# Optimization experiments

Measured on AMD Instinct MI355X. Metric: run time of the kernel, lower is better.

Reference implementation:

```python
import jax, jax.numpy as jnp
import numpy as np

DN = ('NCDHW', 'OIDHW', 'NCDHW')


def conv3d(x, w, b, stride=2, pad=1):
    # w: [Cout, Cin, k, k, k] (PyTorch Conv3d layout == OIDHW)
    y = jax.lax.conv_general_dilated(x, w, (stride,) * 3, [(pad, pad)] * 3,
                                     dimension_numbers=DN)
    return y + b[None, :, None, None, None]


def convT3d(x, w, b, stride=2, pad=1):
    # w: [Cin, Cout, k, k, k] (PyTorch ConvTranspose3d layout).
    # ConvTranspose(k,s,p) == conv(lhs_dilated by s, flipped kernel, pad = k-1-p)
    k = w.shape[2]
    wf = jnp.transpose(jnp.flip(w, (2, 3, 4)), (1, 0, 2, 3, 4))  # -> OIDHW
    p = k - 1 - pad
    y = jax.lax.conv_general_dilated(x, wf, (1, 1, 1), [(p, p)] * 3,
                                     lhs_dilation=(stride,) * 3,
                                     dimension_numbers=DN)
    return y + b[None, :, None, None, None]


def setup_inputs() -> dict:
    key = jax.random.key(0)
    ks = jax.random.split(key, 14)
    s = 0.05
    inp = {
        'x': jax.random.normal(ks[0], (4, 1, 128, 128, 128), jnp.float32),
        # encoder conv weights (OIDHW) + biases
        'w1': jax.random.normal(ks[1], (16, 1, 4, 4, 4), jnp.float32) * s,
        'b1': jnp.zeros((16,), jnp.float32),
        'w2': jax.random.normal(ks[2], (32, 16, 4, 4, 4), jnp.float32) * s,
        'b2': jnp.zeros((32,), jnp.float32),
        'w3': jax.random.normal(ks[3], (64, 32, 4, 4, 4), jnp.float32) * s,
        'b3': jnp.zeros((64,), jnp.float32),
        # VQ codebook [num_embeddings=512, latent_dim=64]
        'codebook': jax.random.normal(ks[4], (512, 64), jnp.float32),
        # decoder conv-transpose weights (PyTorch layout: [Cin, Cout, k,k,k]) + biases
        'dw1': jax.random.normal(ks[5], (64, 32, 4, 4, 4), jnp.float32) * s,
        'db1': jnp.zeros((32,), jnp.float32),
        'dw2': jax.random.normal(ks[6], (32, 16, 4, 4, 4), jnp.float32) * s,
        'db2': jnp.zeros((16,), jnp.float32),
        'dw3': jax.random.normal(ks[7], (16, 1, 4, 4, 4), jnp.float32) * s,
        'db3': jnp.zeros((1,), jnp.float32),
    }
    return inp


def reference(x, w1, b1, w2, b2, w3, b3, codebook, dw1, db1, dw2, db2, dw3, db3):
    # ---- encoder ----
    h = jax.nn.relu(conv3d(x, w1, b1))
    h = jax.nn.relu(conv3d(h, w2, b2))
    z_e = conv3d(h, w3, b3)                      # [B, C=64, D, H, W]
    B, C, D, H, W = z_e.shape

    # ---- vector quantization (cdist + argmin + gather) ----
    zf = jnp.transpose(z_e.reshape(B, C, -1), (0, 2, 1))   # [B, N, C]
    # squared euclidean distances (argmin identical to cdist argmin)
    d2 = (jnp.sum(zf * zf, axis=-1, keepdims=True)
          + jnp.sum(codebook * codebook, axis=-1)[None, None, :]
          - 2.0 * jnp.einsum('bnc,kc->bnk', zf, codebook))  # [B, N, K]
    encoding_indices = jnp.argmin(d2, axis=-1)              # [B, N]
    q = codebook[encoding_indices]                          # [B, N, C]
    quantized = jnp.transpose(q, (0, 2, 1)).reshape(B, C, D, H, W)
    # straight-through estimator
    quantized = z_e + jax.lax.stop_gradient(quantized - z_e)

    # ---- decoder ----
    h = jax.nn.relu(convT3d(quantized, dw1, db1))
    h = jax.nn.relu(convT3d(h, dw2, db2))
    x_hat = jax.nn.sigmoid(convT3d(h, dw3, db3))
    return (x_hat, quantized, z_e)
```

## Files before the change

### kernel.cpp

```cpp
#include <hip/hip_runtime.h>
#include <math.h>


__device__ __forceinline__ float4 ld4(const float* p) {
  float4 q; __builtin_memcpy(&q, p, 16); return q;
}
struct F3 { float x, y, z; };
__device__ __forceinline__ F3 ld3(const float* p) {
  F3 q; __builtin_memcpy(&q, p, 12); return q;
}

#define WAVES_HINT __attribute__((amdgpu_waves_per_eu(2, 4)))

template<int CIN, int COUT>
__global__ __launch_bounds__(256) void k_repackT(const float* __restrict__ w,
                                                 float* __restrict__ dst) {
  const int idx = blockIdx.x * 256 + threadIdx.x;
  if (idx >= CIN * 8 * COUT * 8) return;
  const int a  = idx & 7;
  const int co = (idx >> 3) % COUT;
  const int p  = ((idx >> 3) / COUT) & 7;
  const int ci2 = idx / (8 * COUT * 8);
  const int az = a >> 2, ay = (a >> 1) & 1, ax = a & 1;
  const int pz = p >> 2, py = (p >> 1) & 1, px = p & 1;
  const int kz = 3 - pz - 2 * az, ky = 3 - py - 2 * ay, kx = 3 - px - 2 * ax;
  dst[(((size_t)(ci2 * 8 + p) * COUT + co) * 16) + az * 8 + (ay * 2 + ax)] =
      w[((size_t)ci2 * COUT + co) * 64 + (kz * 16 + ky * 4 + kx)];
}

template<int S, int D, int NCH>
__global__ __launch_bounds__(256) void k_zhalo(float* __restrict__ buf) {
  const int vol = S * S * S;
  const long long idx = (long long)blockIdx.x * 256 + threadIdx.x;
  if (idx >= (long long)NCH * vol) return;
  const int r = (int)(idx % vol);
  const int z = r / (S * S), y = (r / S) % S, x = r % S;
  if (z < 1 || z > D || y < 1 || y > D || x < 1 || x > D) buf[idx] = 0.0f;
}

__global__ __launch_bounds__(256) void k_pad(const float* __restrict__ x,
                                             float* __restrict__ dp) {
  constexpr long long VOL = 130LL * 130 * 130;
  const long long idx = (long long)blockIdx.x * 256 + threadIdx.x;
  if (idx >= 4 * VOL) return;
  const int b = (int)(idx / VOL);
  const int r = (int)(idx % VOL);
  const int z = r / (130 * 130), y = (r / 130) % 130, xx = r % 130;
  float v = 0.0f;
  if (z >= 1 && z <= 128 && y >= 1 && y <= 128 && xx >= 1 && xx <= 128)
    v = x[(((long long)b * 128 + (z - 1)) * 128 + (y - 1)) * 128 + (xx - 1)];
  dp[idx] = v;
}

template<int CIN, int COUT, int DIN, int DOUT, int OCG, int TZ, bool RELU,
         bool INP, int SIN, bool OUTP, int SOUT, int NG>
__global__ __launch_bounds__(256) WAVES_HINT
void k_conv(const float* __restrict__ xin, const float* __restrict__ wg,
            const float* __restrict__ bias, float* __restrict__ out) {
  constexpr int NBX = DOUT / 8, NBY = DOUT / 8, NBZ = DOUT / (4 * TZ);
  constexpr size_t VIN  = INP  ? (size_t)SIN * SIN * SIN : (size_t)DIN * DIN * DIN;
  constexpr size_t VOUT = OUTP ? (size_t)SOUT * SOUT * SOUT : (size_t)DOUT * DOUT * DOUT;
  const int tid = threadIdx.x;
  const int tx = tid & 7, ty = (tid >> 3) & 7, tz = tid >> 6;
  int bb = blockIdx.x;
  const int g  = bb % NG;  bb /= NG;
  const int gx = bb % NBX; bb /= NBX;
  const int gy = bb % NBY; bb /= NBY;
  const int gz = bb % NBZ; bb /= NBZ;
  const int b = bb;
  const int oc0 = g * OCG;
  const int ow = gx * 8 + tx, oh = gy * 8 + ty, od0 = gz * (4 * TZ) + tz;

  float acc[TZ][OCG];
#pragma unroll
  for (int j = 0; j < TZ; ++j)
#pragma unroll
    for (int c = 0; c < OCG; ++c) acc[j][c] = 0.0f;

#pragma unroll 1
  for (int ci = 0; ci < CIN; ++ci) {
    const float* xb = xin + (size_t)(b * CIN + ci) * VIN;
#pragma unroll 1
    for (int t16 = 0; t16 < 16; ++t16) {
      float4 q[TZ];
      if (INP) {
        const int zp = od0 * 2 + (t16 >> 2);
        const int yp = oh * 2 + (t16 & 3);
        const float* r0 = xb + ((size_t)zp * SIN + yp) * SIN + ow * 2;
#pragma unroll
        for (int j = 0; j < TZ; ++j) q[j] = ld4(r0 + (size_t)j * 8 * SIN * SIN);
      } else {
        const int y  = oh * 2 - 1 + (t16 & 3);
        const int x0 = ow * 2 - 1;
        const bool vy = (unsigned)y < (unsigned)DIN;
#pragma unroll
        for (int j = 0; j < TZ; ++j) {
          const int z = od0 * 2 - 1 + (t16 >> 2) + j * 8;
          const bool vz = vy && ((unsigned)z < (unsigned)DIN);
          const float* xr = xb + ((size_t)z * DIN + y) * DIN + x0;
          q[j].x = (vz && (unsigned)(x0 + 0) < (unsigned)DIN) ? xr[0] : 0.0f;
          q[j].y = (vz && (unsigned)(x0 + 1) < (unsigned)DIN) ? xr[1] : 0.0f;
          q[j].z = (vz && (unsigned)(x0 + 2) < (unsigned)DIN) ? xr[2] : 0.0f;
          q[j].w = (vz && (unsigned)(x0 + 3) < (unsigned)DIN) ? xr[3] : 0.0f;
        }
      }
#pragma unroll
      for (int c = 0; c < OCG; ++c) {
        const float4 w4 = ld4(wg + ((size_t)(oc0 + c) * CIN + ci) * 64 + t16 * 4);
#pragma unroll
        for (int j = 0; j < TZ; ++j) {
          acc[j][c] = fmaf(q[j].x, w4.x, acc[j][c]);
          acc[j][c] = fmaf(q[j].y, w4.y, acc[j][c]);
          acc[j][c] = fmaf(q[j].z, w4.z, acc[j][c]);
          acc[j][c] = fmaf(q[j].w, w4.w, acc[j][c]);
        }
      }
    }
  }

#pragma unroll
  for (int c = 0; c < OCG; ++c) {
    const float bv = bias[oc0 + c];
#pragma unroll
    for (int j = 0; j < TZ; ++j) {
      float v = acc[j][c] + bv;
      if (RELU) v = fmaxf(v, 0.0f);
      const int od = od0 + j * 4;
      if (OUTP)
        out[(size_t)(b * COUT + oc0 + c) * VOUT
            + ((size_t)(od + 1) * SOUT + (oh + 1)) * SOUT + (ow + 1)] = v;
      else
        out[(size_t)(b * COUT + oc0 + c) * VOUT
            + ((size_t)od * DOUT + oh) * DOUT + ow] = v;
    }
  }
}

template<int CIN, int COUT, int DIN, int OCG, int TZ, int EPI, int SIN,
         bool OUTP, int SOUT, int NG>
__global__ __launch_bounds__(256) WAVES_HINT
void k_convt(const float* __restrict__ xin, const float* __restrict__ wp,
             const float* __restrict__ bias, float* __restrict__ out) {
  constexpr int DOUT = 2 * DIN, NBX = DIN / 8, NBY = DIN / 8,
                NBZ = DIN / (4 * TZ);
  constexpr size_t VIN  = (size_t)SIN * SIN * SIN;
  constexpr size_t VOUT = OUTP ? (size_t)SOUT * SOUT * SOUT
                               : (size_t)DOUT * DOUT * DOUT;
  const int tid = threadIdx.x;
  const int tx = tid & 7, ty = (tid >> 3) & 7, tz = tid >> 6;
  int bb = blockIdx.x;
  const int g  = bb % NG;  bb /= NG;
  const int gx = bb % NBX; bb /= NBX;
  const int gy = bb % NBY; bb /= NBY;
  const int gz = bb % NBZ; bb /= NBZ;
  const int b = bb;
  const int oc0 = g * OCG;
  const int mx = gx * 8 + tx, my = gy * 8 + ty;
  const int mz0 = gz * (4 * TZ) + tz * TZ;

  float acc[TZ][8][OCG];
#pragma unroll
  for (int j = 0; j < TZ; ++j)
#pragma unroll
    for (int p = 0; p < 8; ++p)
#pragma unroll
      for (int c = 0; c < OCG; ++c) acc[j][p][c] = 0.0f;

#pragma unroll 1
  for (int ci = 0; ci < CIN; ++ci) {
    const float* xb = xin + (size_t)(b * CIN + ci) * VIN
                          + ((size_t)mz0 * SIN + my) * SIN + mx;
    float xn[TZ + 2][3][3];
#pragma unroll
    for (int dz = 0; dz < TZ + 2; ++dz)
#pragma unroll
      for (int dy = 0; dy < 3; ++dy) {
        const F3 t = ld3(xb + ((size_t)dz * SIN + dy) * SIN);
        xn[dz][dy][0] = t.x; xn[dz][dy][1] = t.y; xn[dz][dy][2] = t.z;
      }
    __builtin_amdgcn_sched_barrier(0);

    const float* wci = wp + (size_t)ci * 8 * COUT * 16;
#pragma unroll
    for (int p = 0; p < 8; ++p) {
      const int pz = p >> 2, py = (p >> 1) & 1, px = p & 1;
#pragma unroll
      for (int c = 0; c < OCG; ++c) {
        const float* wb = wci + ((size_t)p * COUT + (oc0 + c)) * 16;
        const float4 wA = ld4(wb);
        const float4 wB = ld4(wb + 8);
#pragma unroll
        for (int j = 0; j < TZ; ++j)
          acc[j][p][c] = fmaf(xn[j + pz][py    ][px    ], wA.x, acc[j][p][c]);
#pragma unroll
        for (int j = 0; j < TZ; ++j)
          acc[j][p][c] = fmaf(xn[j + pz][py    ][px + 1], wA.y, acc[j][p][c]);
#pragma unroll
        for (int j = 0; j < TZ; ++j)
          acc[j][p][c] = fmaf(xn[j + pz][py + 1][px    ], wA.z, acc[j][p][c]);
#pragma unroll
        for (int j = 0; j < TZ; ++j)
          acc[j][p][c] = fmaf(xn[j + pz][py + 1][px + 1], wA.w, acc[j][p][c]);
#pragma unroll
        for (int j = 0; j < TZ; ++j)
          acc[j][p][c] = fmaf(xn[j + pz + 1][py    ][px    ], wB.x, acc[j][p][c]);
#pragma unroll
        for (int j = 0; j < TZ; ++j)
          acc[j][p][c] = fmaf(xn[j + pz + 1][py    ][px + 1], wB.y, acc[j][p][c]);
#pragma unroll
        for (int j = 0; j < TZ; ++j)
          acc[j][p][c] = fmaf(xn[j + pz + 1][py + 1][px    ], wB.z, acc[j][p][c]);
#pragma unroll
        for (int j = 0; j < TZ; ++j)
          acc[j][p][c] = fmaf(xn[j + pz + 1][py + 1][px + 1], wB.w, acc[j][p][c]);
      }
    }
  }

#pragma unroll
  for (int c = 0; c < OCG; ++c) {
    const float bv = bias[oc0 + c];
#pragma unroll
    for (int j = 0; j < TZ; ++j) {
      const int mz = mz0 + j;
#pragma unroll
      for (int p = 0; p < 8; ++p) {
        const int pz = p >> 2, py = (p >> 1) & 1, px = p & 1;
        float v = acc[j][p][c] + bv;
        if (EPI == 1) v = fmaxf(v, 0.0f);
        if (EPI == 2) v = 1.0f / (1.0f + expf(-v));
        if (OUTP)
          out[(size_t)(b * COUT + oc0 + c) * VOUT
              + ((size_t)(2 * mz + pz + 1) * SOUT + (2 * my + py + 1)) * SOUT
              + (2 * mx + px + 1)] = v;
        else
          out[(size_t)(b * COUT + oc0 + c) * VOUT
              + ((size_t)(2 * mz + pz) * DOUT + (2 * my + py)) * DOUT
              + (2 * mx + px)] = v;
      }
    }
  }
}

__global__ __launch_bounds__(256) void k_vq(const float* __restrict__ ze,
                                            const float* __restrict__ cb,
                                            float* __restrict__ quant,
                                            float* __restrict__ quantp) {
  __shared__ float ct[64 * 65];
  __shared__ float zs[4][64];
  __shared__ int   bis[4];
  const int tid  = threadIdx.x;
  const int lane = tid & 63;
  const int wv   = tid >> 6;
  const int p0 = blockIdx.x * 4;
  const int b  = p0 >> 12;
  const int n0 = p0 & 4095;

  {
    const int c = tid >> 2, j = tid & 3;
    zs[j][c] = ze[((size_t)(b * 64 + c) << 12) + n0 + j];
  }

  float best = 3.4e38f;
  int bi = 0;
#pragma unroll 1
  for (int ch = 0; ch < 8; ++ch) {
    __syncthreads();
    for (int i = tid; i < 4096; i += 256) {
      const int r = i >> 6, c = i & 63;
      ct[r * 65 + c] = cb[((ch * 64 + r) << 6) + c];
    }
    __syncthreads();
    float d = 0.0f;
#pragma unroll 8
    for (int c = 0; c < 64; ++c) {
      const float t = zs[wv][c] - ct[lane * 65 + c];
      d = fmaf(t, t, d);
    }
    const int k = ch * 64 + lane;
    if (d < best) { best = d; bi = k; }
  }
#pragma unroll
  for (int off = 32; off > 0; off >>= 1) {
    const float ob = __shfl_down(best, off);
    const int   oi = __shfl_down(bi, off);
    if (ob < best || (ob == best && oi < bi)) { best = ob; bi = oi; }
  }
  if (lane == 0) bis[wv] = bi;
  __syncthreads();
  {
    const int c = tid >> 2, j = tid & 3;
    const float val = cb[(bis[j] << 6) + c];
    const int n = n0 + j;
    quant[((size_t)(b * 64 + c) << 12) + n] = val;
    const int zz = n >> 8, yy = (n >> 4) & 15, xx = n & 15;
    quantp[(size_t)(b * 64 + c) * 8000
           + ((size_t)(zz + 1) * 20 + (yy + 1)) * 20 + (xx + 1)] = val;
  }
}

extern "C" void kernel_launch(void* const* d_in, const int* in_sizes, int n_in,
                              void* d_out, int out_size, void* d_ws, size_t ws_size,
                              hipStream_t stream) {
  const float* x   = (const float*)d_in[0];
  const float* w1  = (const float*)d_in[1];
  const float* b1  = (const float*)d_in[2];
  const float* w2  = (const float*)d_in[3];
  const float* b2  = (const float*)d_in[4];
  const float* w3  = (const float*)d_in[5];
  const float* b3  = (const float*)d_in[6];
  const float* cb  = (const float*)d_in[7];
  const float* dw1 = (const float*)d_in[8];
  const float* db1 = (const float*)d_in[9];
  const float* dw2 = (const float*)d_in[10];
  const float* db2 = (const float*)d_in[11];
  const float* dw3 = (const float*)d_in[12];
  const float* db3 = (const float*)d_in[13];

  float* outf  = (float*)d_out;
  float* xhat  = outf;
  float* quant = outf + 8388608;
  float* ze    = outf + 9437184;

  float* dp = outf;

  float* regA = (float*)d_ws;
  float* regB = regA + (size_t)64 * 68 * 68 * 68;
  float* regC = regB + (size_t)128 * 36 * 36 * 36;
  float* t1p = regC + (size_t)256 * 20 * 20 * 20;
  float* t2p = t1p + 262144;
  float* t3p = t2p + 65536;

  k_repackT<64, 32><<<512, 256, 0, stream>>>(dw1, t1p);
  k_repackT<32, 16><<<128, 256, 0, stream>>>(dw2, t2p);
  k_repackT<16, 1><<<4, 256, 0, stream>>>(dw3, t3p);
  k_zhalo<68, 64, 64><<<78608, 256, 0, stream>>>(regA);
  k_zhalo<36, 32, 128><<<23328, 256, 0, stream>>>(regB);
  k_zhalo<20, 16, 256><<<8000, 256, 0, stream>>>(regC);
  k_pad<<<34329, 256, 0, stream>>>(x, dp);

  k_conv<1, 16, 128, 64, 16, 2, true, true, 130, true, 68, 1>
      <<<2048, 256, 0, stream>>>(dp, w1, b1, regA);
  k_conv<16, 32, 64, 32, 16, 1, true, true, 68, true, 36, 2>
      <<<1024, 256, 0, stream>>>(regA, w2, b2, regB);
  k_conv<32, 64, 32, 16, 4, 1, false, true, 36, false, 16, 16>
      <<<1024, 256, 0, stream>>>(regB, w3, b3, ze);
  k_vq<<<4096, 256, 0, stream>>>(ze, cb, quant, regC);
  k_convt<64, 32, 16, 2, 1, 1, 20, true, 36, 16>
      <<<1024, 256, 0, stream>>>(regC, t1p, db1, regB);
  k_convt<32, 16, 32, 2, 4, 1, 36, true, 68, 8>
      <<<1024, 256, 0, stream>>>(regB, t2p, db2, regA);
  k_convt<16, 1, 64, 1, 4, 2, 68, false, 0, 1>
      <<<1024, 256, 0, stream>>>(regA, t3p, db3, xhat);
}
```

Before: 1.060 ms.

## Stage conv and convT weights through double-buffered LDS with register prefetch

Both the strided conv and transposed conv kernels now copy each input channel's weight slice into shared memory once per block, with the next slice prefetched into registers while the current one is consumed. The inner loops then read weights from LDS instead of issuing per-thread global loads for the same uniform data. The cost is two block-wide barriers per input channel and extra LDS use, which may limit occupancy or stall waves.

```diff
diff --git a/kernel.cpp b/kernel.cpp
--- a/kernel.cpp
+++ b/kernel.cpp
@@ -60,6 +60,11 @@
   constexpr int NBX = DOUT / 8, NBY = DOUT / 8, NBZ = DOUT / (4 * TZ);
   constexpr size_t VIN  = INP  ? (size_t)SIN * SIN * SIN : (size_t)DIN * DIN * DIN;
   constexpr size_t VOUT = OUTP ? (size_t)SOUT * SOUT * SOUT : (size_t)DOUT * DOUT * DOUT;
+  constexpr int NBUF = (CIN > 1) ? 2 : 1;
+  constexpr int WPT  = (OCG * 64) / 256;
+  static_assert(WPT == 4 || WPT == 1, "OCG must be 16 or 4");
+  __shared__ float wlds[NBUF][OCG][64];
+
   const int tid = threadIdx.x;
   const int tx = tid & 7, ty = (tid >> 3) & 7, tz = tid >> 6;
   int bb = blockIdx.x;
@@ -71,14 +76,32 @@
   const int oc0 = g * OCG;
   const int ow = gx * 8 + tx, oh = gy * 8 + ty, od0 = gz * (4 * TZ) + tz;
 
+  const int s_oc  = (WPT == 4) ? (tid >> 4) : (tid >> 6);
+  const int s_off = (WPT == 4) ? ((tid & 15) << 2) : (tid & 63);
+
   float acc[TZ][OCG];
 #pragma unroll
   for (int j = 0; j < TZ; ++j)
 #pragma unroll
     for (int c = 0; c < OCG; ++c) acc[j][c] = 0.0f;
+
+  {
+    const float* src = wg + ((size_t)(oc0 + s_oc) * CIN + 0) * 64 + s_off;
+    if (WPT == 4) *(float4*)&wlds[0][s_oc][s_off] = ld4(src);
+    else          wlds[0][s_oc][s_off] = *src;
+  }
+  __syncthreads();
 
 #pragma unroll 1
   for (int ci = 0; ci < CIN; ++ci) {
+    float4 wpf4; float wpf1;
+    const bool pf = (CIN > 1) && (ci + 1 < CIN);
+    if (pf) {
+      const float* src = wg + ((size_t)(oc0 + s_oc) * CIN + (ci + 1)) * 64 + s_off;
+      if (WPT == 4) wpf4 = ld4(src); else wpf1 = *src;
+    }
+    const int cur = (CIN > 1) ? (ci & 1) : 0;
+
     const float* xb = xin + (size_t)(b * CIN + ci) * VIN;
 #pragma unroll 1
     for (int t16 = 0; t16 < 16; ++t16) {
@@ -106,7 +129,7 @@
       }
 #pragma unroll
       for (int c = 0; c < OCG; ++c) {
-        const float4 w4 = ld4(wg + ((size_t)(oc0 + c) * CIN + ci) * 64 + t16 * 4);
+        const float4 w4 = *(const float4*)&wlds[cur][c][t16 * 4];
 #pragma unroll
         for (int j = 0; j < TZ; ++j) {
           acc[j][c] = fmaf(q[j].x, w4.x, acc[j][c]);
@@ -115,6 +138,15 @@
           acc[j][c] = fmaf(q[j].w, w4.w, acc[j][c]);
         }
       }
+    }
+
+    if (CIN > 1) {
+      __syncthreads();
+      if (pf) {
+        if (WPT == 4) *(float4*)&wlds[cur ^ 1][s_oc][s_off] = wpf4;
+        else          wlds[cur ^ 1][s_oc][s_off] = wpf1;
+      }
+      __syncthreads();
     }
   }
 
@@ -146,6 +178,10 @@
   constexpr size_t VIN  = (size_t)SIN * SIN * SIN;
   constexpr size_t VOUT = OUTP ? (size_t)SOUT * SOUT * SOUT
                                : (size_t)DOUT * DOUT * DOUT;
+  constexpr int SL = 8 * OCG * 16;
+  static_assert(SL <= 256, "slice must fit one stage round");
+  __shared__ float wl[2][8][OCG][16];
+
   const int tid = threadIdx.x;
   const int tx = tid & 7, ty = (tid >> 3) & 7, tz = tid >> 6;
   int bb = blockIdx.x;
@@ -158,6 +194,11 @@
   const int mx = gx * 8 + tx, my = gy * 8 + ty;
   const int mz0 = gz * (4 * TZ) + tz * TZ;
 
+  const int s_p = tid / (OCG * 16);
+  const int s_c = (tid >> 4) % OCG;
+  const int s_f = tid & 15;
+  const float* wbase = wp + ((size_t)s_p * COUT + (oc0 + s_c)) * 16 + s_f;
+
   float acc[TZ][8][OCG];
 #pragma unroll
   for (int j = 0; j < TZ; ++j)
@@ -165,9 +206,17 @@
     for (int p = 0; p < 8; ++p)
 #pragma unroll
       for (int c = 0; c < OCG; ++c) acc[j][p][c] = 0.0f;
+
+  if (tid < SL) wl[0][s_p][s_c][s_f] = wbase[0];
+  __syncthreads();
 
 #pragma unroll 1
   for (int ci = 0; ci < CIN; ++ci) {
+    float wpf;
+    const bool pf = (ci + 1 < CIN);
+    if (pf && tid < SL) wpf = wbase[(size_t)(ci + 1) * 8 * COUT * 16];
+    const int cur = ci & 1;
+
     const float* xb = xin + (size_t)(b * CIN + ci) * VIN
                           + ((size_t)mz0 * SIN + my) * SIN + mx;
     float xn[TZ + 2][3][3];
@@ -180,15 +229,13 @@
       }
     __builtin_amdgcn_sched_barrier(0);
 
-    const float* wci = wp + (size_t)ci * 8 * COUT * 16;
 #pragma unroll
     for (int p = 0; p < 8; ++p) {
       const int pz = p >> 2, py = (p >> 1) & 1, px = p & 1;
 #pragma unroll
       for (int c = 0; c < OCG; ++c) {
-        const float* wb = wci + ((size_t)p * COUT + (oc0 + c)) * 16;
-        const float4 wA = ld4(wb);
-        const float4 wB = ld4(wb + 8);
+        const float4 wA = *(const float4*)&wl[cur][p][c][0];
+        const float4 wB = *(const float4*)&wl[cur][p][c][8];
 #pragma unroll
         for (int j = 0; j < TZ; ++j)
           acc[j][p][c] = fmaf(xn[j + pz][py    ][px    ], wA.x, acc[j][p][c]);
@@ -215,6 +262,10 @@
           acc[j][p][c] = fmaf(xn[j + pz + 1][py + 1][px + 1], wB.w, acc[j][p][c]);
       }
     }
+
+    __syncthreads();
+    if (pf && tid < SL) wl[cur ^ 1][s_p][s_c][s_f] = wpf;
+    __syncthreads();
   }
 
 #pragma unroll
```

Result: slower. 1.123 ms (+5.9%).
